# Optimization experiments

Measured on AMD Instinct MI355X. Metric: run time of the kernel, lower is better.

## Reference

```python
import jax, jax.numpy as jnp
import numpy as np

NUM_CAPSULE = 10
DIM_CAPSULE = 16
NUM_ROUTING = 3
EPS = 1e-7  # tf.keras.backend.epsilon()


def squash(v, axis=-1):
    s2 = jnp.sum(jnp.square(v), axis=axis, keepdims=True)
    scale = s2 / (1.0 + s2) / jnp.sqrt(s2 + EPS)
    return scale * v


def setup_inputs() -> dict:
    key = jax.random.key(0)
    k1, k2 = jax.random.split(key)
    B, in_dim = 16384, 2048
    inputs = jax.random.normal(k1, (B, in_dim), dtype=jnp.float32)
    # glorot-uniform-ish scale for the kernel
    limit = np.sqrt(6.0 / (in_dim + NUM_CAPSULE * DIM_CAPSULE)).astype(np.float32)
    kernel = jax.random.uniform(k2, (in_dim, NUM_CAPSULE * DIM_CAPSULE),
                                dtype=jnp.float32, minval=-limit, maxval=limit)
    return {"inputs": inputs, "kernel": kernel}


def reference(inputs, kernel):
    B = inputs.shape[0]
    # [B, in_dim] @ [in_dim, nc*dc] -> [B, nc, dc]
    inputs_hat = (inputs @ kernel).reshape(B, NUM_CAPSULE, DIM_CAPSULE)
    b = jnp.zeros((B, NUM_CAPSULE, 1), dtype=inputs.dtype)
    outputs = None
    for _ in range(NUM_ROUTING):
        c = jax.nn.softmax(b, axis=1)                      # [B, nc, 1]
        s = jnp.sum(c * inputs_hat, axis=1, keepdims=True)  # [B, 1, dc]
        outputs = squash(s)                                 # [B, 1, dc]
        # matmul(inputs_hat, outputs, transpose_b=True) -> [B, nc, 1]
        b = b + jnp.einsum('bnd,bd->bn', inputs_hat, outputs[:, 0, :])[:, :, None]
    return outputs[:, 0, :]  # [B, dc]
```

## Files before the change

### kernel.cpp

```cpp
#include <hip/hip_runtime.h>

typedef unsigned int u32;
typedef unsigned short u16;
typedef __attribute__((ext_vector_type(8))) __bf16 bf16x8;
typedef __attribute__((ext_vector_type(4))) float f32x4;

#define N_CAP 10
#define D_CAP 16
#define NN 160
#define KK 2048
#define BM 64
#define NSTEPS 64
#define THREADS 704
#define HAT_STRIDE 165
#define BSTEP 20480
#define ATILE 8192
#define NBUF 4

__device__ __align__(16) unsigned char Wpack_g[NSTEPS * BSTEP];

__device__ __forceinline__ u32 pack_hi(float f0, float f1) {
  return __builtin_amdgcn_perm(__builtin_bit_cast(u32, f1),
                               __builtin_bit_cast(u32, f0), 0x07060302u);
}
__device__ __forceinline__ float hi_part(float f) {
  u32 u = __builtin_bit_cast(u32, f) & 0xFFFF0000u;
  return __builtin_bit_cast(float, u);
}
union U4B8 { uint4 u; bf16x8 b; };

__device__ __forceinline__ void split2(const float4& x, const float4& y,
                                       bf16x8& h, bf16x8& l) {
  U4B8 hh, ll;
  hh.u.x = pack_hi(x.x, x.y); hh.u.y = pack_hi(x.z, x.w);
  hh.u.z = pack_hi(y.x, y.y); hh.u.w = pack_hi(y.z, y.w);
  float l0 = x.x - hi_part(x.x), l1 = x.y - hi_part(x.y);
  float l2 = x.z - hi_part(x.z), l3 = x.w - hi_part(x.w);
  float l4 = y.x - hi_part(y.x), l5 = y.y - hi_part(y.y);
  float l6 = y.z - hi_part(y.z), l7 = y.w - hi_part(y.w);
  ll.u.x = pack_hi(l0, l1); ll.u.y = pack_hi(l2, l3);
  ll.u.z = pack_hi(l4, l5); ll.u.w = pack_hi(l6, l7);
  h = hh.b; l = ll.b;
}

__device__ __forceinline__ void mfma12(bf16x8 ah0, bf16x8 al0, bf16x8 ah1,
                                       bf16x8 al1, uint4 b0, uint4 b1, uint4 b2,
                                       uint4 b3, f32x4& a00, f32x4& a01,
                                       f32x4& a10, f32x4& a11) {
  U4B8 u0, u1, u2, u3;
  u0.u = b0; u1.u = b1; u2.u = b2; u3.u = b3;
  a00 = __builtin_amdgcn_mfma_f32_16x16x32_bf16(ah0, u0.b, a00, 0, 0, 0);
  a00 = __builtin_amdgcn_mfma_f32_16x16x32_bf16(ah0, u2.b, a00, 0, 0, 0);
  a00 = __builtin_amdgcn_mfma_f32_16x16x32_bf16(al0, u0.b, a00, 0, 0, 0);
  a01 = __builtin_amdgcn_mfma_f32_16x16x32_bf16(ah0, u1.b, a01, 0, 0, 0);
  a01 = __builtin_amdgcn_mfma_f32_16x16x32_bf16(ah0, u3.b, a01, 0, 0, 0);
  a01 = __builtin_amdgcn_mfma_f32_16x16x32_bf16(al0, u1.b, a01, 0, 0, 0);
  a10 = __builtin_amdgcn_mfma_f32_16x16x32_bf16(ah1, u0.b, a10, 0, 0, 0);
  a10 = __builtin_amdgcn_mfma_f32_16x16x32_bf16(ah1, u2.b, a10, 0, 0, 0);
  a10 = __builtin_amdgcn_mfma_f32_16x16x32_bf16(al1, u0.b, a10, 0, 0, 0);
  a11 = __builtin_amdgcn_mfma_f32_16x16x32_bf16(ah1, u1.b, a11, 0, 0, 0);
  a11 = __builtin_amdgcn_mfma_f32_16x16x32_bf16(ah1, u3.b, a11, 0, 0, 0);
  a11 = __builtin_amdgcn_mfma_f32_16x16x32_bf16(al1, u1.b, a11, 0, 0, 0);
}

__global__ void pack_w(const float* __restrict__ W) {
  const int tid = blockIdx.x * 256 + threadIdx.x;
  if (tid >= NSTEPS * 5 * 64 * 4) return;
  const int v = tid & 3;
  const int lane = (tid >> 2) & 63;
  const int sw = tid >> 8;
  const int wjp = sw % 5;
  const int s = sw / 5;
  const int col = 32 * wjp + 16 * (v & 1) + (lane & 15);
  const int kb = 32 * s + 8 * (lane >> 4);
  u32 r[4];
#pragma unroll
  for (int jj = 0; jj < 4; ++jj) {
    float x0 = W[(size_t)(kb + 2 * jj) * NN + col];
    float x1 = W[(size_t)(kb + 2 * jj + 1) * NN + col];
    if (v >= 2) { x0 -= hi_part(x0); x1 -= hi_part(x1); }
    r[jj] = pack_hi(x0, x1);
  }
  uint4 o; o.x = r[0]; o.y = r[1]; o.z = r[2]; o.w = r[3];
  *(uint4*)(Wpack_g + (size_t)tid * 16) = o;
}

#define GLOAD(gp, lp) __builtin_amdgcn_global_load_lds( \
    (const __attribute__((address_space(1))) u32*)(gp), \
    (__attribute__((address_space(3))) u32*)(lp), 16, 0, 0)
#define BARRIER() asm volatile("s_barrier" ::: "memory")

__global__ __launch_bounds__(THREADS, 1) void capsule_fused(
    const float* __restrict__ X, float* __restrict__ out) {
  __shared__ __align__(16) char AsA[NBUF * ATILE];
  __shared__ __align__(16) float hat[BM * HAT_STRIDE];

  const int t = threadIdx.x;
  const int rbase = blockIdx.x * BM;
  const int lane = t & 63;
  const int w = t >> 6;

  if (w == 10) {
    const float* g0 = X + (size_t)(rbase + (lane >> 3)) * KK
                        + (size_t)(((lane & 7) ^ (lane >> 3)) * 4);
#define STAGE(S, BV) do {                                         \
    const float* ga_ = g0 + (size_t)(S) * 32;                     \
    char* la_ = AsA + (BV) * ATILE;                               \
    GLOAD(ga_,           la_);                                    \
    GLOAD(ga_ +  8 * KK, la_ + 1024);                             \
    GLOAD(ga_ + 16 * KK, la_ + 2048);                             \
    GLOAD(ga_ + 24 * KK, la_ + 3072);                             \
    GLOAD(ga_ + 32 * KK, la_ + 4096);                             \
    GLOAD(ga_ + 40 * KK, la_ + 5120);                             \
    GLOAD(ga_ + 48 * KK, la_ + 6144);                             \
    GLOAD(ga_ + 56 * KK, la_ + 7168);                             \
  } while (0)
    STAGE(0, 0);
    STAGE(1, 1);
    asm volatile("s_waitcnt vmcnt(0)" ::: "memory");
    BARRIER();
    STAGE(2, 2);
    BARRIER();
#pragma unroll 1
    for (int i = 0; i < NSTEPS; ++i) {
      if (i + 3 < NSTEPS) {
        STAGE(i + 3, (i + 3) & 3);
        asm volatile("s_waitcnt vmcnt(8)" ::: "memory");
      } else {
        asm volatile("s_waitcnt vmcnt(0)" ::: "memory");
      }
      BARRIER();
    }
#undef STAGE
  } else {
    const int wip = (w >= 5) ? 1 : 0;
    const int wjp = w - 5 * wip;
    const int l15 = lane & 15;
    const int q = lane >> 4;
    const int r0 = 32 * wip + l15;
    const int r1 = r0 + 16;
    const int c0 = 2 * q, c1 = 2 * q + 1;
    const int o00 = (r0 >> 3) * 1024 + (r0 & 7) * 128 + ((c0 ^ (r0 & 7)) << 4);
    const int o01 = (r0 >> 3) * 1024 + (r0 & 7) * 128 + ((c1 ^ (r0 & 7)) << 4);
    const int o10 = (r1 >> 3) * 1024 + (r1 & 7) * 128 + ((c0 ^ (r1 & 7)) << 4);
    const int o11 = (r1 >> 3) * 1024 + (r1 & 7) * 128 + ((c1 ^ (r1 & 7)) << 4);
    const unsigned char* pB = Wpack_g + ((size_t)wjp * 64 + lane) * 64;

    f32x4 acc00 = {0.f,0.f,0.f,0.f}, acc01 = {0.f,0.f,0.f,0.f};
    f32x4 acc10 = {0.f,0.f,0.f,0.f}, acc11 = {0.f,0.f,0.f,0.f};

    float4 A00a, A01a, A10a, A11a, A00b, A01b, A10b, A11b;
    uint4 Bc0, Bc1, Bc2, Bc3, Bn0, Bn1, Bn2, Bn3;

#define READSET(SFX, SLOT) do {                                   \
    const char* ca_ = AsA + (SLOT) * ATILE;                       \
    A00##SFX = *(const float4*)(ca_ + o00);                       \
    A01##SFX = *(const float4*)(ca_ + o01);                       \
    A10##SFX = *(const float4*)(ca_ + o10);                       \
    A11##SFX = *(const float4*)(ca_ + o11);                       \
  } while (0)

#define BLOADC(P0, P1, P2, P3, S) do {                            \
    const uint4* bp_ = (const uint4*)(pB + (size_t)(S) * BSTEP);  \
    P0 = bp_[0]; P1 = bp_[1]; P2 = bp_[2]; P3 = bp_[3];           \
  } while (0)

#define COMPUTE(SFX, P0, P1, P2, P3) do {                         \
    bf16x8 ah0, al0, ah1, al1;                                    \
    split2(A00##SFX, A01##SFX, ah0, al0);                         \
    split2(A10##SFX, A11##SFX, ah1, al1);                         \
    __builtin_amdgcn_s_setprio(1);                                \
    mfma12(ah0, al0, ah1, al1, P0, P1, P2, P3,                    \
           acc00, acc01, acc10, acc11);                           \
    __builtin_amdgcn_s_setprio(0);                                \
  } while (0)

    BLOADC(Bc0, Bc1, Bc2, Bc3, 0);
    BARRIER();
    READSET(a, 0);
    BARRIER();
    int ni = 1;
#pragma unroll 1
    for (int ii = 0; ii < NSTEPS / 2; ++ii) {
      BLOADC(Bn0, Bn1, Bn2, Bn3, 2 * ii + 1);
      READSET(b, ni);
      ni = (ni + 1) & 3;
      COMPUTE(a, Bc0, Bc1, Bc2, Bc3);
      BARRIER();
      BLOADC(Bc0, Bc1, Bc2, Bc3, (2 * ii + 2) & (NSTEPS - 1));
      if (ii != NSTEPS / 2 - 1) {
        READSET(a, ni);
        ni = (ni + 1) & 3;
      }
      COMPUTE(b, Bn0, Bn1, Bn2, Bn3);
      BARRIER();
    }
#undef READSET
#undef BLOADC
#undef COMPUTE

#pragma unroll
    for (int r = 0; r < 4; ++r) {
      const int rowb = 32 * wip + 4 * q + r;
      const int colb = 32 * wjp + l15;
      hat[rowb * HAT_STRIDE + colb]             = acc00[r];
      hat[rowb * HAT_STRIDE + colb + 16]        = acc01[r];
      hat[(rowb + 16) * HAT_STRIDE + colb]      = acc10[r];
      hat[(rowb + 16) * HAT_STRIDE + colb + 16] = acc11[r];
    }
  }
  __syncthreads();

  if (t < BM * 8) {
    const int r = t >> 3;
    const int d0 = t & 7;
    float h0[N_CAP], h1[N_CAP];
#pragma unroll
    for (int n = 0; n < N_CAP; ++n) {
      h0[n] = hat[r * HAT_STRIDE + n * D_CAP + d0];
      h1[n] = hat[r * HAT_STRIDE + n * D_CAP + d0 + 8];
    }
    float bb[N_CAP];
#pragma unroll
    for (int n = 0; n < N_CAP; ++n) bb[n] = 0.f;
    float v0 = 0.f, v1 = 0.f;
#pragma unroll
    for (int it = 0; it < 3; ++it) {
      float mx = bb[0];
#pragma unroll
      for (int n = 1; n < N_CAP; ++n) mx = fmaxf(mx, bb[n]);
      float c[N_CAP], se = 0.f;
#pragma unroll
      for (int n = 0; n < N_CAP; ++n) { c[n] = __expf(bb[n] - mx); se += c[n]; }
      const float inv = 1.f / se;
      float s0 = 0.f, s1 = 0.f;
#pragma unroll
      for (int n = 0; n < N_CAP; ++n) { s0 += c[n] * h0[n]; s1 += c[n] * h1[n]; }
      s0 *= inv; s1 *= inv;
      float s2 = s0 * s0 + s1 * s1;
      s2 += __shfl_xor(s2, 1);
      s2 += __shfl_xor(s2, 2);
      s2 += __shfl_xor(s2, 4);
      const float scale = s2 / ((1.f + s2) * sqrtf(s2 + 1e-7f));
      v0 = scale * s0; v1 = scale * s1;
      if (it < 2) {
#pragma unroll
        for (int n = 0; n < N_CAP; ++n) {
          float dd = h0[n] * v0 + h1[n] * v1;
          dd += __shfl_xor(dd, 1);
          dd += __shfl_xor(dd, 2);
          dd += __shfl_xor(dd, 4);
          bb[n] += dd;
        }
      }
    }
    out[(size_t)(rbase + r) * D_CAP + d0] = v0;
    out[(size_t)(rbase + r) * D_CAP + d0 + 8] = v1;
  }
}

extern "C" void kernel_launch(void* const* d_in, const int* in_sizes, int n_in,
                              void* d_out, int out_size, void* d_ws, size_t ws_size,
                              hipStream_t stream) {
  const float* X = (const float*)d_in[0];
  const float* W = (const float*)d_in[1];
  if (n_in >= 2 && in_sizes[0] == KK * NN) {
    X = (const float*)d_in[1];
    W = (const float*)d_in[0];
  }
  (void)d_ws; (void)ws_size; (void)out_size;
  pack_w<<<(NSTEPS * 5 * 64 * 4 + 255) / 256, 256, 0, stream>>>(W);
  capsule_fused<<<16384 / BM, THREADS, 0, stream>>>(X, (float*)d_out);
}
```

Measured before the change: 212.6 us.

## Split fused capsule kernel into split-K GEMM and separate routing kernel

Replaces the single fused kernel, which used a dedicated loader wave and a 4-deep LDS ring for 64-row tiles, with a split-K=2 GEMM over 32-row tiles. The GEMM uses 320-thread blocks at up to 4 blocks per CU and simple double buffering. Partial results are written to a workspace in global memory, and a second kernel sums the two partials and runs the routing iterations. The aim is more blocks and better occupancy to hide latency. In exchange it adds a global round trip for the 16384x160 partial hat matrices twice, plus an extra kernel launch.

```diff
diff --git a/kernel.cpp b/kernel.cpp
--- a/kernel.cpp
+++ b/kernel.cpp
@@ -9,13 +9,13 @@
 #define D_CAP 16
 #define NN 160
 #define KK 2048
-#define BM 64
 #define NSTEPS 64
-#define THREADS 704
-#define HAT_STRIDE 165
+#define SPLITK 2
+#define LSTEPS 32
+#define BMR 32
+#define GTHREADS 320
 #define BSTEP 20480
-#define ATILE 8192
-#define NBUF 4
+#define HATN (16384 * NN)
 
 __device__ __align__(16) unsigned char Wpack_g[NSTEPS * BSTEP];
 
@@ -88,175 +88,136 @@
 #define GLOAD(gp, lp) __builtin_amdgcn_global_load_lds( \
     (const __attribute__((address_space(1))) u32*)(gp), \
     (__attribute__((address_space(3))) u32*)(lp), 16, 0, 0)
-#define BARRIER() asm volatile("s_barrier" ::: "memory")
-
-__global__ __launch_bounds__(THREADS, 1) void capsule_fused(
-    const float* __restrict__ X, float* __restrict__ out) {
-  __shared__ __align__(16) char AsA[NBUF * ATILE];
-  __shared__ __align__(16) float hat[BM * HAT_STRIDE];
+
+__global__ __launch_bounds__(GTHREADS, 4) void capsule_gemm(
+    const float* __restrict__ X, float* __restrict__ hp) {
+  __shared__ __align__(16) char As[2][BMR * 128];
 
   const int t = threadIdx.x;
-  const int rbase = blockIdx.x * BM;
   const int lane = t & 63;
-  const int w = t >> 6;
-
-  if (w == 10) {
-    const float* g0 = X + (size_t)(rbase + (lane >> 3)) * KK
-                        + (size_t)(((lane & 7) ^ (lane >> 3)) * 4);
-#define STAGE(S, BV) do {                                         \
-    const float* ga_ = g0 + (size_t)(S) * 32;                     \
-    char* la_ = AsA + (BV) * ATILE;                               \
-    GLOAD(ga_,           la_);                                    \
-    GLOAD(ga_ +  8 * KK, la_ + 1024);                             \
-    GLOAD(ga_ + 16 * KK, la_ + 2048);                             \
-    GLOAD(ga_ + 24 * KK, la_ + 3072);                             \
-    GLOAD(ga_ + 32 * KK, la_ + 4096);                             \
-    GLOAD(ga_ + 40 * KK, la_ + 5120);                             \
-    GLOAD(ga_ + 48 * KK, la_ + 6144);                             \
-    GLOAD(ga_ + 56 * KK, la_ + 7168);                             \
-  } while (0)
-    STAGE(0, 0);
-    STAGE(1, 1);
-    asm volatile("s_waitcnt vmcnt(0)" ::: "memory");
-    BARRIER();
-    STAGE(2, 2);
-    BARRIER();
-#pragma unroll 1
-    for (int i = 0; i < NSTEPS; ++i) {
-      if (i + 3 < NSTEPS) {
-        STAGE(i + 3, (i + 3) & 3);
-        asm volatile("s_waitcnt vmcnt(8)" ::: "memory");
-      } else {
-        asm volatile("s_waitcnt vmcnt(0)" ::: "memory");
-      }
-      BARRIER();
-    }
-#undef STAGE
-  } else {
-    const int wip = (w >= 5) ? 1 : 0;
-    const int wjp = w - 5 * wip;
-    const int l15 = lane & 15;
-    const int q = lane >> 4;
-    const int r0 = 32 * wip + l15;
-    const int r1 = r0 + 16;
-    const int c0 = 2 * q, c1 = 2 * q + 1;
-    const int o00 = (r0 >> 3) * 1024 + (r0 & 7) * 128 + ((c0 ^ (r0 & 7)) << 4);
-    const int o01 = (r0 >> 3) * 1024 + (r0 & 7) * 128 + ((c1 ^ (r0 & 7)) << 4);
-    const int o10 = (r1 >> 3) * 1024 + (r1 & 7) * 128 + ((c0 ^ (r1 & 7)) << 4);
-    const int o11 = (r1 >> 3) * 1024 + (r1 & 7) * 128 + ((c1 ^ (r1 & 7)) << 4);
-    const unsigned char* pB = Wpack_g + ((size_t)wjp * 64 + lane) * 64;
-
-    f32x4 acc00 = {0.f,0.f,0.f,0.f}, acc01 = {0.f,0.f,0.f,0.f};
-    f32x4 acc10 = {0.f,0.f,0.f,0.f}, acc11 = {0.f,0.f,0.f,0.f};
-
-    float4 A00a, A01a, A10a, A11a, A00b, A01b, A10b, A11b;
-    uint4 Bc0, Bc1, Bc2, Bc3, Bn0, Bn1, Bn2, Bn3;
-
-#define READSET(SFX, SLOT) do {                                   \
-    const char* ca_ = AsA + (SLOT) * ATILE;                       \
-    A00##SFX = *(const float4*)(ca_ + o00);                       \
-    A01##SFX = *(const float4*)(ca_ + o01);                       \
-    A10##SFX = *(const float4*)(ca_ + o10);                       \
-    A11##SFX = *(const float4*)(ca_ + o11);                       \
-  } while (0)
+  const int wjp = t >> 6;
+  const int ks = blockIdx.x & 1;
+  const int rbase = (blockIdx.x >> 1) * BMR;
+
+  const int srow = t >> 3;
+  const int schk = (t & 7) ^ (srow & 7);
+  const float* gA = X + (size_t)(rbase + srow) * KK + ks * (LSTEPS * 32)
+                      + schk * 4;
+
+  const int l15 = lane & 15;
+  const int q = lane >> 4;
+  const int r0 = l15, r1 = l15 + 16;
+  const int c0 = 2 * q, c1 = 2 * q + 1;
+  const int o00 = (r0 >> 3) * 1024 + (r0 & 7) * 128 + ((c0 ^ (r0 & 7)) << 4);
+  const int o01 = (r0 >> 3) * 1024 + (r0 & 7) * 128 + ((c1 ^ (r0 & 7)) << 4);
+  const int o10 = (r1 >> 3) * 1024 + (r1 & 7) * 128 + ((c0 ^ (r1 & 7)) << 4);
+  const int o11 = (r1 >> 3) * 1024 + (r1 & 7) * 128 + ((c1 ^ (r1 & 7)) << 4);
+  const unsigned char* pB = Wpack_g
+      + (((size_t)(ks * LSTEPS) * 5 + wjp) * 64 + lane) * 64;
+
+  f32x4 acc00 = {0.f,0.f,0.f,0.f}, acc01 = {0.f,0.f,0.f,0.f};
+  f32x4 acc10 = {0.f,0.f,0.f,0.f}, acc11 = {0.f,0.f,0.f,0.f};
+  uint4 Bc0, Bc1, Bc2, Bc3, Bn0, Bn1, Bn2, Bn3;
 
 #define BLOADC(P0, P1, P2, P3, S) do {                            \
     const uint4* bp_ = (const uint4*)(pB + (size_t)(S) * BSTEP);  \
     P0 = bp_[0]; P1 = bp_[1]; P2 = bp_[2]; P3 = bp_[3];           \
   } while (0)
 
-#define COMPUTE(SFX, P0, P1, P2, P3) do {                         \
+#define AMFMA(BUF, P0, P1, P2, P3) do {                           \
+    const char* ca_ = As[BUF];                                    \
+    float4 A00 = *(const float4*)(ca_ + o00);                     \
+    float4 A01 = *(const float4*)(ca_ + o01);                     \
+    float4 A10 = *(const float4*)(ca_ + o10);                     \
+    float4 A11 = *(const float4*)(ca_ + o11);                     \
     bf16x8 ah0, al0, ah1, al1;                                    \
-    split2(A00##SFX, A01##SFX, ah0, al0);                         \
-    split2(A10##SFX, A11##SFX, ah1, al1);                         \
-    __builtin_amdgcn_s_setprio(1);                                \
+    split2(A00, A01, ah0, al0);                                   \
+    split2(A10, A11, ah1, al1);                                   \
     mfma12(ah0, al0, ah1, al1, P0, P1, P2, P3,                    \
            acc00, acc01, acc10, acc11);                           \
-    __builtin_amdgcn_s_setprio(0);                                \
   } while (0)
 
-    BLOADC(Bc0, Bc1, Bc2, Bc3, 0);
-    BARRIER();
-    READSET(a, 0);
-    BARRIER();
-    int ni = 1;
+  if (t < 256) GLOAD(gA, As[0] + t * 16);
+  BLOADC(Bc0, Bc1, Bc2, Bc3, 0);
+  __syncthreads();
+
 #pragma unroll 1
-    for (int ii = 0; ii < NSTEPS / 2; ++ii) {
-      BLOADC(Bn0, Bn1, Bn2, Bn3, 2 * ii + 1);
-      READSET(b, ni);
-      ni = (ni + 1) & 3;
-      COMPUTE(a, Bc0, Bc1, Bc2, Bc3);
-      BARRIER();
-      BLOADC(Bc0, Bc1, Bc2, Bc3, (2 * ii + 2) & (NSTEPS - 1));
-      if (ii != NSTEPS / 2 - 1) {
-        READSET(a, ni);
-        ni = (ni + 1) & 3;
-      }
-      COMPUTE(b, Bn0, Bn1, Bn2, Bn3);
-      BARRIER();
+  for (int ii = 0; ii < LSTEPS / 2; ++ii) {
+    if (t < 256) GLOAD(gA + (size_t)(2 * ii + 1) * 32, As[1] + t * 16);
+    BLOADC(Bn0, Bn1, Bn2, Bn3, 2 * ii + 1);
+    AMFMA(0, Bc0, Bc1, Bc2, Bc3);
+    __syncthreads();
+    if (ii != LSTEPS / 2 - 1) {
+      if (t < 256) GLOAD(gA + (size_t)(2 * ii + 2) * 32, As[0] + t * 16);
+      BLOADC(Bc0, Bc1, Bc2, Bc3, 2 * ii + 2);
     }
-#undef READSET
+    AMFMA(1, Bn0, Bn1, Bn2, Bn3);
+    __syncthreads();
+  }
 #undef BLOADC
-#undef COMPUTE
-
-#pragma unroll
-    for (int r = 0; r < 4; ++r) {
-      const int rowb = 32 * wip + 4 * q + r;
-      const int colb = 32 * wjp + l15;
-      hat[rowb * HAT_STRIDE + colb]             = acc00[r];
-      hat[rowb * HAT_STRIDE + colb + 16]        = acc01[r];
-      hat[(rowb + 16) * HAT_STRIDE + colb]      = acc10[r];
-      hat[(rowb + 16) * HAT_STRIDE + colb + 16] = acc11[r];
-    }
-  }
-  __syncthreads();
-
-  if (t < BM * 8) {
-    const int r = t >> 3;
-    const int d0 = t & 7;
-    float h0[N_CAP], h1[N_CAP];
-#pragma unroll
-    for (int n = 0; n < N_CAP; ++n) {
-      h0[n] = hat[r * HAT_STRIDE + n * D_CAP + d0];
-      h1[n] = hat[r * HAT_STRIDE + n * D_CAP + d0 + 8];
-    }
-    float bb[N_CAP];
-#pragma unroll
-    for (int n = 0; n < N_CAP; ++n) bb[n] = 0.f;
-    float v0 = 0.f, v1 = 0.f;
-#pragma unroll
-    for (int it = 0; it < 3; ++it) {
-      float mx = bb[0];
-#pragma unroll
-      for (int n = 1; n < N_CAP; ++n) mx = fmaxf(mx, bb[n]);
-      float c[N_CAP], se = 0.f;
-#pragma unroll
-      for (int n = 0; n < N_CAP; ++n) { c[n] = __expf(bb[n] - mx); se += c[n]; }
-      const float inv = 1.f / se;
-      float s0 = 0.f, s1 = 0.f;
-#pragma unroll
-      for (int n = 0; n < N_CAP; ++n) { s0 += c[n] * h0[n]; s1 += c[n] * h1[n]; }
-      s0 *= inv; s1 *= inv;
-      float s2 = s0 * s0 + s1 * s1;
-      s2 += __shfl_xor(s2, 1);
-      s2 += __shfl_xor(s2, 2);
-      s2 += __shfl_xor(s2, 4);
-      const float scale = s2 / ((1.f + s2) * sqrtf(s2 + 1e-7f));
-      v0 = scale * s0; v1 = scale * s1;
-      if (it < 2) {
-#pragma unroll
-        for (int n = 0; n < N_CAP; ++n) {
-          float dd = h0[n] * v0 + h1[n] * v1;
-          dd += __shfl_xor(dd, 1);
-          dd += __shfl_xor(dd, 2);
-          dd += __shfl_xor(dd, 4);
-          bb[n] += dd;
-        }
+#undef AMFMA
+
+  float* hb = hp + (size_t)ks * HATN;
+#pragma unroll
+  for (int r = 0; r < 4; ++r) {
+    const int rowb = 4 * q + r;
+    const int colb = 32 * wjp + l15;
+    hb[(size_t)(rbase + rowb) * NN + colb]           = acc00[r];
+    hb[(size_t)(rbase + rowb) * NN + colb + 16]      = acc01[r];
+    hb[(size_t)(rbase + rowb + 16) * NN + colb]      = acc10[r];
+    hb[(size_t)(rbase + rowb + 16) * NN + colb + 16] = acc11[r];
+  }
+}
+
+__global__ __launch_bounds__(256) void capsule_route(
+    const float* __restrict__ hp, float* __restrict__ out) {
+  const int gid = blockIdx.x * 256 + threadIdx.x;
+  const int r = gid >> 3;
+  const int d0 = gid & 7;
+  const float* h0p = hp + (size_t)r * NN;
+  const float* h1p = h0p + HATN;
+  float h0[N_CAP], h1[N_CAP];
+#pragma unroll
+  for (int n = 0; n < N_CAP; ++n) {
+    h0[n] = h0p[n * D_CAP + d0]     + h1p[n * D_CAP + d0];
+    h1[n] = h0p[n * D_CAP + d0 + 8] + h1p[n * D_CAP + d0 + 8];
+  }
+  float bb[N_CAP];
+#pragma unroll
+  for (int n = 0; n < N_CAP; ++n) bb[n] = 0.f;
+  float v0 = 0.f, v1 = 0.f;
+#pragma unroll
+  for (int it = 0; it < 3; ++it) {
+    float mx = bb[0];
+#pragma unroll
+    for (int n = 1; n < N_CAP; ++n) mx = fmaxf(mx, bb[n]);
+    float c[N_CAP], se = 0.f;
+#pragma unroll
+    for (int n = 0; n < N_CAP; ++n) { c[n] = __expf(bb[n] - mx); se += c[n]; }
+    const float inv = 1.f / se;
+    float s0 = 0.f, s1 = 0.f;
+#pragma unroll
+    for (int n = 0; n < N_CAP; ++n) { s0 += c[n] * h0[n]; s1 += c[n] * h1[n]; }
+    s0 *= inv; s1 *= inv;
+    float s2 = s0 * s0 + s1 * s1;
+    s2 += __shfl_xor(s2, 1);
+    s2 += __shfl_xor(s2, 2);
+    s2 += __shfl_xor(s2, 4);
+    const float scale = s2 / ((1.f + s2) * sqrtf(s2 + 1e-7f));
+    v0 = scale * s0; v1 = scale * s1;
+    if (it < 2) {
+#pragma unroll
+      for (int n = 0; n < N_CAP; ++n) {
+        float dd = h0[n] * v0 + h1[n] * v1;
+        dd += __shfl_xor(dd, 1);
+        dd += __shfl_xor(dd, 2);
+        dd += __shfl_xor(dd, 4);
+        bb[n] += dd;
       }
     }
-    out[(size_t)(rbase + r) * D_CAP + d0] = v0;
-    out[(size_t)(rbase + r) * D_CAP + d0 + 8] = v1;
-  }
+  }
+  out[(size_t)r * D_CAP + d0] = v0;
+  out[(size_t)r * D_CAP + d0 + 8] = v1;
 }
 
 extern "C" void kernel_launch(void* const* d_in, const int* in_sizes, int n_in,
@@ -268,7 +229,9 @@
     X = (const float*)d_in[1];
     W = (const float*)d_in[0];
   }
-  (void)d_ws; (void)ws_size; (void)out_size;
+  (void)out_size; (void)ws_size;
+  float* hp = (float*)d_ws;
   pack_w<<<(NSTEPS * 5 * 64 * 4 + 255) / 256, 256, 0, stream>>>(W);
-  capsule_fused<<<16384 / BM, THREADS, 0, stream>>>(X, (float*)d_out);
-}
+  capsule_gemm<<<(16384 / BMR) * SPLITK, GTHREADS, 0, stream>>>(X, hp);
+  capsule_route<<<16384 * 8 / 256, 256, 0, stream>>>(hp, (float*)d_out);
+}
```

Result: slower. 250.5 us (+17.8%).
